# Kernel tuning notes

Hardware: AMD Instinct MI355X
Metric: run time of the kernel (lower is better)

## Reference

```python
import jax, jax.numpy as jnp
import numpy as np


def _gru_dir(x, kernel, rec_kernel, bias):
    """Keras GRU (reset_after=True). x: [B,T,D] -> [B,T,U]."""
    B, T, D = x.shape
    U = rec_kernel.shape[0]
    # Precompute input projections for all timesteps: [B,T,3U]
    xw = jnp.einsum('btd,dk->btk', x, kernel) + bias[0]
    h0 = jnp.zeros((B, U), dtype=x.dtype)

    def step(h, xw_t):
        rec = h @ rec_kernel + bias[1]            # [B,3U]
        xz, xr, xh = jnp.split(xw_t, 3, axis=-1)
        rz, rr, rh = jnp.split(rec, 3, axis=-1)
        z = jax.nn.sigmoid(xz + rz)
        r = jax.nn.sigmoid(xr + rr)
        hh = jnp.tanh(xh + r * rh)
        h_new = z * h + (1.0 - z) * hh
        return h_new, h_new

    _, hs = jax.lax.scan(step, h0, jnp.swapaxes(xw, 0, 1))  # hs: [T,B,U]
    return jnp.swapaxes(hs, 0, 1)


def setup_inputs() -> dict:
    key = jax.random.key(0)
    ks = jax.random.split(key, 7)
    B, T, D, U = 64, 1024, 256, 256
    s_in = 1.0 / np.sqrt(D)
    s_rec = 1.0 / np.sqrt(U)
    return {
        'x': jax.random.normal(ks[0], (B, T, D), jnp.float32),
        'kernel_f': jax.random.normal(ks[1], (D, 3 * U), jnp.float32) * s_in,
        'rec_kernel_f': jax.random.normal(ks[2], (U, 3 * U), jnp.float32) * s_rec,
        'bias_f': jnp.zeros((2, 3 * U), jnp.float32),
        'kernel_b': jax.random.normal(ks[3], (D, 3 * U), jnp.float32) * s_in,
        'rec_kernel_b': jax.random.normal(ks[4], (U, 3 * U), jnp.float32) * s_rec,
        'bias_b': jnp.zeros((2, 3 * U), jnp.float32),
    }


def reference(x, kernel_f, rec_kernel_f, bias_f, kernel_b, rec_kernel_b, bias_b):
    # Forward direction
    out_f = _gru_dir(x, kernel_f, rec_kernel_f, bias_f)
    # Backward direction: reverse time, run GRU, reverse output back
    xb = x[:, ::-1, :]
    out_b = _gru_dir(xb, kernel_b, rec_kernel_b, bias_b)[:, ::-1, :]
    # Bidirectional merge_mode='concat'
    return jnp.concatenate([out_f, out_b], axis=-1)  # [B,T,2U]
```

## Files before the change

### kernel.cpp

```cpp
#include <hip/hip_runtime.h>
#include <hip/hip_fp16.h>
#include <hip/hip_bf16.h>

typedef __attribute__((ext_vector_type(8))) short bf16x8;
typedef __attribute__((ext_vector_type(4))) float f32x4;

__device__ __forceinline__ short f2bf(float f) {
    unsigned u = __builtin_bit_cast(unsigned, f);
    unsigned r = (u + 0x7FFFu + ((u >> 16) & 1u)) >> 16;
    return (short)r;
}
__device__ __forceinline__ float fast_rcp(float x) {
    return __builtin_amdgcn_rcpf(x);
}
__device__ __forceinline__ float fast_exp(float x) {
    return __builtin_amdgcn_exp2f(x * 1.4426950408889634f);
}

__global__ __launch_bounds__(256) void prep_kernel(
    const float* __restrict__ kf, const float* __restrict__ kb,
    const float* __restrict__ rf, const float* __restrict__ rb,
    short* __restrict__ kT, short* __restrict__ rTf, short* __restrict__ rTb)
{
    int idx = blockIdx.x * 256 + threadIdx.x;
    int n = idx >> 8;
    int k = idx & 255;
    const float* src = (n < 768) ? kf : kb;
    int nn = (n < 768) ? n : (n - 768);
    kT[idx] = f2bf(src[k * 768 + nn]);
    if (n < 768) {
        rTf[idx] = f2bf(rf[k * 768 + n]);
        rTb[idx] = f2bf(rb[k * 768 + n]);
    }
}

__global__ __launch_bounds__(256) void proj_kernel(
    const float* __restrict__ x, const short* __restrict__ kT,
    const float* __restrict__ bias_f, const float* __restrict__ bias_b,
    char* __restrict__ xwp_f, char* __restrict__ xwp_b)
{
    __shared__ short lA[64][264];
    __shared__ short lB[128][264];

    const int tid = threadIdx.x;
    const int m0 = blockIdx.x * 64;
    const int n0 = blockIdx.y * 128;

    const int b_blk  = m0 >> 10;
    const int bg     = b_blk >> 4;
    const int rowg   = b_blk & 15;
    const int hi_t   = rowg >> 2;
    const int i_t    = rowg & 3;
    const int tbase  = m0 & 1023;

#pragma unroll
    for (int rep = 0; rep < 16; ++rep) {
        int lin = rep * 256 + tid;
        int r = lin >> 6;
        int c4 = lin & 63;
        float4 v = *(const float4*)(x + (size_t)(m0 + r) * 256 + c4 * 4);
        short4 s;
        s.x = f2bf(v.x); s.y = f2bf(v.y); s.z = f2bf(v.z); s.w = f2bf(v.w);
        *(short4*)&lA[r][c4 * 4] = s;
    }
#pragma unroll
    for (int rep = 0; rep < 16; ++rep) {
        int lin = rep * 256 + tid;
        int r = lin >> 5;
        int c8 = lin & 31;
        uint4 v = *(const uint4*)(kT + (size_t)(n0 + r) * 256 + c8 * 8);
        *(uint4*)&lB[r][c8 * 8] = v;
    }
    __syncthreads();

    const int w = tid >> 6, l = tid & 63;
    const int l15 = l & 15, hi = l >> 4;

    bf16x8 a[8];
#pragma unroll
    for (int kt = 0; kt < 8; ++kt)
        a[kt] = *(const bf16x8*)&lA[w * 16 + l15][kt * 32 + hi * 8];

#pragma unroll
    for (int j = 0; j < 8; ++j) {
        f32x4 acc = {0.f, 0.f, 0.f, 0.f};
#pragma unroll
        for (int kt = 0; kt < 8; ++kt) {
            bf16x8 b = *(const bf16x8*)&lB[j * 16 + l15][kt * 32 + hi * 8];
            acc = __builtin_amdgcn_mfma_f32_16x16x32_bf16(a[kt], b, acc, 0, 0, 0);
        }
        int ng = n0 + j * 16 + l15;
        int dirb = ng >= 768;
        int nn = ng - (dirb ? 768 : 0);
        const float* bias = dirb ? bias_b : bias_f;
        float badd = bias[nn] + ((nn < 512) ? bias[768 + nn] : 0.f);
        char* basep = dirb ? xwp_b : xwp_f;

        int g   = nn >> 8;
        int cg2 = nn & 255;
        int wt  = cg2 >> 4;
        int lane_t = hi_t * 16 + (cg2 & 15);

#pragma unroll
        for (int i = 0; i < 4; ++i) {
            int t = tbase + w * 16 + hi * 4 + i;
            unsigned short hv = __builtin_bit_cast(unsigned short,
                                    __float2half(acc[i] + badd));
            if (g < 2) {
                *(unsigned short*)(basep + ((size_t)bg << 24) + ((size_t)t << 14)
                                   + (wt << 10) + (lane_t << 4) + ((g * 4 + i_t) << 1)) = hv;
            } else {
                *(unsigned short*)(basep + 67108864u + ((size_t)bg << 23) + ((size_t)t << 13)
                                   + (wt << 9) + (lane_t << 3) + (i_t << 1)) = hv;
            }
        }
    }
}

#define GRU_STEP(PR, PW)                                                     \
  {                                                                          \
    uint4  xv16 = *(const uint4*)xp16;  xp16 += step16;                      \
    uint2  xv8  = *(const uint2*)xp8;   xp8  += step8;                       \
    unsigned bbase = 0;                                                      \
    asm volatile("" : "+v"(bbase));    \
    f32x4 az = {0.f,0.f,0.f,0.f}, ar = {0.f,0.f,0.f,0.f},                    \
          ah = {0.f,0.f,0.f,0.f};                                            \
    _Pragma("unroll") for (int kt = 0; kt < 8; ++kt) {                       \
      bf16x8 aq = *(const bf16x8*)((const char*)hfrag + (PR)*8192            \
                                   + kt * 1024 + l * 16);                    \
      bf16x8 bh;                                                             \
      if (kt < 5) bh = Bh[kt];                                               \
      else bh = *(const bf16x8*)((const char*)bfrag + bbase                  \
                                 + (kt - 5) * 16384 + w * 1024 + l * 16);    \
      az = __builtin_amdgcn_mfma_f32_16x16x32_bf16(aq, Bz[kt], az, 0,0,0);   \
      ar = __builtin_amdgcn_mfma_f32_16x16x32_bf16(aq, Br[kt], ar, 0,0,0);   \
      ah = __builtin_amdgcn_mfma_f32_16x16x32_bf16(aq, bh, ah, 0,0,0);       \
    }                                                                        \
    const __half* hx  = (const __half*)&xv16;                                \
    const __half* hx8 = (const __half*)&xv8;                                 \
    float hn[4];                                                             \
    _Pragma("unroll") for (int i = 0; i < 4; ++i) {                          \
      float zi  = fast_rcp(1.f + fast_exp(-(__half2float(hx[i]) + az[i])));  \
      float rri = fast_rcp(1.f + fast_exp(-(__half2float(hx[4+i]) + ar[i])));\
      float pre = __half2float(hx8[i]) + rri * (ah[i] + b1h);                \
      float sg  = fast_rcp(1.f + fast_exp(-2.f * pre));                      \
      float hh  = 2.f * sg - 1.f;                                            \
      float h2  = hh + zi * (hold[i] - hh);                                  \
      hold[i] = h2;  hn[i] = h2;                                             \
      opbase[i * 524288] = h2;                                               \
    }                                                                        \
    unsigned pk0, pk1;                                                       \
    asm("v_cvt_pk_bf16_f32 %0, %1, %2" : "=v"(pk0) : "v"(hn[0]), "v"(hn[1]));\
    asm("v_cvt_pk_bf16_f32 %0, %1, %2" : "=v"(pk1) : "v"(hn[2]), "v"(hn[3]));\
    {                                                                        \
      char* hb = (char*)hfrag + (PW)*8192 + wb;                              \
      *(short*)(hb)      = (short)(pk0 & 0xffff);                            \
      *(short*)(hb + 16) = (short)(pk0 >> 16);                               \
      *(short*)(hb + 32) = (short)(pk1 & 0xffff);                            \
      *(short*)(hb + 48) = (short)(pk1 >> 16);                               \
    }                                                                        \
    opbase += ostep;                                                         \
    asm volatile("s_waitcnt lgkmcnt(0)\n\ts_barrier" ::: "memory");          \
  }

__global__ __launch_bounds__(1024) void gru_kernel(
    const char* __restrict__ xwp_f, const char* __restrict__ xwp_b,
    const short* __restrict__ recT_f, const short* __restrict__ recT_b,
    const float* __restrict__ bias_f, const float* __restrict__ bias_b,
    float* __restrict__ out)
{
    __shared__ short hfrag[2][8][64][8];
    __shared__ short bfrag[3][16][64][8];

    const int tid = threadIdx.x;
    const int w = tid >> 6, l = tid & 63;
    const int l15 = l & 15, hi = l >> 4;
    const int dir = blockIdx.x >> 2;
    const int bg  = blockIdx.x & 3;
    const int b0  = bg * 16;

    const char*  xwp  = dir ? xwp_b  : xwp_f;
    const short* recT = dir ? recT_b : recT_f;
    const float* bias = dir ? bias_b : bias_f;

    const int cg = w * 16 + l15;
    const float b1h = bias[768 + 512 + cg];

    ((int4*)hfrag)[tid] = make_int4(0, 0, 0, 0);

    const char* recTc = (const char*)recT;
    unsigned offz = (((unsigned)(cg)       * 256u) + hi * 8u) * 2u;
    unsigned offr = (((unsigned)(256 + cg) * 256u) + hi * 8u) * 2u;
    unsigned offh = (((unsigned)(512 + cg) * 256u) + hi * 8u) * 2u;
    bf16x8 Bz[8], Br[8], Bh[5];
#pragma unroll
    for (int kt = 0; kt < 8; ++kt) {
        Bz[kt] = *(const bf16x8*)(recTc + offz + kt * 64);
        Br[kt] = *(const bf16x8*)(recTc + offr + kt * 64);
    }
#pragma unroll
    for (int kt = 0; kt < 5; ++kt)
        Bh[kt] = *(const bf16x8*)(recTc + offh + kt * 64);
#pragma unroll
    for (int kt = 5; kt < 8; ++kt) {
        bf16x8 tmp = *(const bf16x8*)(recTc + offh + kt * 64);
        *(bf16x8*)((char*)bfrag + (kt - 5) * 16384 + w * 1024 + l * 16) = tmp;
    }

    const int t0 = dir ? 1023 : 0;
    const long step16 = dir ? -16384 : 16384;
    const long step8  = dir ? -8192  : 8192;
    const char* xp16 = xwp + ((size_t)bg << 24) + ((size_t)t0 << 14)
                       + (w << 10) + (l << 4);
    const char* xp8  = xwp + 67108864u + ((size_t)bg << 23) + ((size_t)t0 << 13)
                       + (w << 9) + (l << 3);

    const long ostep = dir ? -512 : 512;
    float* opbase = out + (size_t)(b0 + hi * 4) * 524288 + (size_t)t0 * 512
                    + (size_t)dir * 256 + cg;

    const unsigned wb = (unsigned)(cg >> 5) * 1024u
                      + ((((unsigned)cg >> 3) & 3u) * 16u) * 16u
                      + (unsigned)(hi * 4) * 16u + ((unsigned)(l15 & 7)) * 2u;

    f32x4 hold = {0.f, 0.f, 0.f, 0.f};
    __syncthreads();

    for (int su = 0; su < 512; ++su) {
        GRU_STEP(0, 1)
        GRU_STEP(1, 0)
    }
}

extern "C" void kernel_launch(void* const* d_in, const int* in_sizes, int n_in,
                              void* d_out, int out_size, void* d_ws, size_t ws_size,
                              hipStream_t stream) {
    const float* x   = (const float*)d_in[0];
    const float* kf  = (const float*)d_in[1];
    const float* rf  = (const float*)d_in[2];
    const float* bf_ = (const float*)d_in[3];
    const float* kb  = (const float*)d_in[4];
    const float* rb  = (const float*)d_in[5];
    const float* bb_ = (const float*)d_in[6];

    char* ws = (char*)d_ws;
    char* xwp_f = ws;
    char* xwp_b = ws + 100663296;
    short* rTf  = (short*)(ws + 201326592);
    short* rTb  = (short*)(ws + 201719808);
    short* kT   = (short*)(ws + 202113024);
    float* out  = (float*)d_out;

    hipLaunchKernelGGL(prep_kernel, dim3(1536), dim3(256), 0, stream,
                       kf, kb, rf, rb, kT, rTf, rTb);
    hipLaunchKernelGGL(proj_kernel, dim3(1024, 12), dim3(256), 0, stream,
                       x, kT, bf_, bb_, xwp_f, xwp_b);
    hipLaunchKernelGGL(gru_kernel, dim3(8), dim3(1024), 0, stream,
                       xwp_f, xwp_b, rTf, rTb, bf_, bb_, out);
}
```

Baseline: 1.867 ms.

## Split each GRU recurrence across two workgroups exchanging hidden state via global flags

Each direction/batch-group recurrence now runs on two 512-thread workgroups, each owning half of the hidden units. The full recurrent weight slice sits in registers, which removes the LDS-staged weight fragments. Each step, a block publishes its bf16 half of h to global memory and raises an atomic flag. The partner spin-waits on that flag, then loads the other half of h for the remaining MFMAs. This halves per-block matmul work and doubles the number of CUs used, at the cost of a cross-CU global-memory handshake on every one of the 1024 serial steps.

New measurement: 4.594 ms. 146% more time.

```diff
diff --git a/kernel.cpp b/kernel.cpp
--- a/kernel.cpp
+++ b/kernel.cpp
@@ -117,28 +117,45 @@
     }
 }
 
-#define GRU_STEP(PR, PW)                                                     \
+#define GRU_STEP(PR, PW, RSLOT, PSLOT)                                       \
   {                                                                          \
     uint4  xv16 = *(const uint4*)xp16;  xp16 += step16;                      \
     uint2  xv8  = *(const uint2*)xp8;   xp8  += step8;                       \
-    unsigned bbase = 0;                                                      \
-    asm volatile("" : "+v"(bbase));    \
     f32x4 az = {0.f,0.f,0.f,0.f}, ar = {0.f,0.f,0.f,0.f},                    \
           ah = {0.f,0.f,0.f,0.f};                                            \
-    _Pragma("unroll") for (int kt = 0; kt < 8; ++kt) {                       \
-      bf16x8 aq = *(const bf16x8*)((const char*)hfrag + (PR)*8192            \
-                                   + kt * 1024 + l * 16);                    \
-      bf16x8 bh;                                                             \
-      if (kt < 5) bh = Bh[kt];                                               \
-      else bh = *(const bf16x8*)((const char*)bfrag + bbase                  \
-                                 + (kt - 5) * 16384 + w * 1024 + l * 16);    \
-      az = __builtin_amdgcn_mfma_f32_16x16x32_bf16(aq, Bz[kt], az, 0,0,0);   \
-      ar = __builtin_amdgcn_mfma_f32_16x16x32_bf16(aq, Br[kt], ar, 0,0,0);   \
-      ah = __builtin_amdgcn_mfma_f32_16x16x32_bf16(aq, bh, ah, 0,0,0);       \
+    _Pragma("unroll") for (int ko = 0; ko < 4; ++ko) {                       \
+      bf16x8 aq = *(const bf16x8*)((const char*)hfrag + (PR)*4096            \
+                                   + ko * 1024 + l * 16);                    \
+      az = __builtin_amdgcn_mfma_f32_16x16x32_bf16(aq, BzO[ko], az, 0,0,0);  \
+      ar = __builtin_amdgcn_mfma_f32_16x16x32_bf16(aq, BrO[ko], ar, 0,0,0);  \
+      ah = __builtin_amdgcn_mfma_f32_16x16x32_bf16(aq, BhO[ko], ah, 0,0,0);  \
+    }                                                                        \
+    if (s > 0) {                                                             \
+      while (__hip_atomic_load(flagp, __ATOMIC_ACQUIRE,                      \
+                               __HIP_MEMORY_SCOPE_AGENT) < s)                \
+        __builtin_amdgcn_s_sleep(1);                                         \
+      const char* rb = pubR + (RSLOT)*4096 + l15 * 256 + hi * 16;            \
+      bf16x8 ra0 = *(const bf16x8*)(rb);                                     \
+      bf16x8 ra1 = *(const bf16x8*)(rb + 64);                                \
+      bf16x8 ra2 = *(const bf16x8*)(rb + 128);                               \
+      bf16x8 ra3 = *(const bf16x8*)(rb + 192);                               \
+      az = __builtin_amdgcn_mfma_f32_16x16x32_bf16(ra0, BzR[0], az, 0,0,0);  \
+      ar = __builtin_amdgcn_mfma_f32_16x16x32_bf16(ra0, BrR[0], ar, 0,0,0);  \
+      ah = __builtin_amdgcn_mfma_f32_16x16x32_bf16(ra0, BhR[0], ah, 0,0,0);  \
+      az = __builtin_amdgcn_mfma_f32_16x16x32_bf16(ra1, BzR[1], az, 0,0,0);  \
+      ar = __builtin_amdgcn_mfma_f32_16x16x32_bf16(ra1, BrR[1], ar, 0,0,0);  \
+      ah = __builtin_amdgcn_mfma_f32_16x16x32_bf16(ra1, BhR[1], ah, 0,0,0);  \
+      az = __builtin_amdgcn_mfma_f32_16x16x32_bf16(ra2, BzR[2], az, 0,0,0);  \
+      ar = __builtin_amdgcn_mfma_f32_16x16x32_bf16(ra2, BrR[2], ar, 0,0,0);  \
+      ah = __builtin_amdgcn_mfma_f32_16x16x32_bf16(ra2, BhR[2], ah, 0,0,0);  \
+      az = __builtin_amdgcn_mfma_f32_16x16x32_bf16(ra3, BzR[3], az, 0,0,0);  \
+      ar = __builtin_amdgcn_mfma_f32_16x16x32_bf16(ra3, BrR[3], ar, 0,0,0);  \
+      ah = __builtin_amdgcn_mfma_f32_16x16x32_bf16(ra3, BhR[3], ah, 0,0,0);  \
     }                                                                        \
     const __half* hx  = (const __half*)&xv16;                                \
     const __half* hx8 = (const __half*)&xv8;                                 \
     float hn[4];                                                             \
+    char* pubw = pubMe + (PSLOT)*4096 + (hi * 4) * 256 + col_rel * 2;        \
     _Pragma("unroll") for (int i = 0; i < 4; ++i) {                          \
       float zi  = fast_rcp(1.f + fast_exp(-(__half2float(hx[i]) + az[i])));  \
       float rri = fast_rcp(1.f + fast_exp(-(__half2float(hx[4+i]) + ar[i])));\
@@ -148,42 +165,52 @@
       float h2  = hh + zi * (hold[i] - hh);                                  \
       hold[i] = h2;  hn[i] = h2;                                             \
       opbase[i * 524288] = h2;                                               \
+      *(short*)(pubw + i * 256) = f2bf(h2);                                  \
     }                                                                        \
     unsigned pk0, pk1;                                                       \
     asm("v_cvt_pk_bf16_f32 %0, %1, %2" : "=v"(pk0) : "v"(hn[0]), "v"(hn[1]));\
     asm("v_cvt_pk_bf16_f32 %0, %1, %2" : "=v"(pk1) : "v"(hn[2]), "v"(hn[3]));\
     {                                                                        \
-      char* hb = (char*)hfrag + (PW)*8192 + wb;                              \
+      char* hb = (char*)hfrag + (PW)*4096 + wb;                              \
       *(short*)(hb)      = (short)(pk0 & 0xffff);                            \
       *(short*)(hb + 16) = (short)(pk0 >> 16);                               \
       *(short*)(hb + 32) = (short)(pk1 & 0xffff);                            \
       *(short*)(hb + 48) = (short)(pk1 >> 16);                               \
     }                                                                        \
     opbase += ostep;                                                         \
-    asm volatile("s_waitcnt lgkmcnt(0)\n\ts_barrier" ::: "memory");          \
+    __syncthreads();              \
+    if (tid == 0)                                                            \
+      __hip_atomic_store(flagMe, s + 1, __ATOMIC_RELEASE,                    \
+                         __HIP_MEMORY_SCOPE_AGENT);                          \
+    ++s;                                                                     \
   }
 
-__global__ __launch_bounds__(1024) void gru_kernel(
+__global__ __launch_bounds__(512) void gru_kernel(
     const char* __restrict__ xwp_f, const char* __restrict__ xwp_b,
     const short* __restrict__ recT_f, const short* __restrict__ recT_b,
     const float* __restrict__ bias_f, const float* __restrict__ bias_b,
+    char* __restrict__ hpub, int* __restrict__ flags,
     float* __restrict__ out)
 {
-    __shared__ short hfrag[2][8][64][8];
-    __shared__ short bfrag[3][16][64][8];
+    __shared__ short hfrag[2][4][64][8];
 
     const int tid = threadIdx.x;
     const int w = tid >> 6, l = tid & 63;
     const int l15 = l & 15, hi = l >> 4;
-    const int dir = blockIdx.x >> 2;
-    const int bg  = blockIdx.x & 3;
-    const int b0  = bg * 16;
+    const int bid  = blockIdx.x;
+    const int half = bid >> 3;
+    const int dir  = (bid >> 2) & 1;
+    const int bg   = bid & 3;
+    const int b0   = bg * 16;
+    const int c0   = half * 128;
+    const int pbid = bid ^ 8;
 
     const char*  xwp  = dir ? xwp_b  : xwp_f;
     const short* recT = dir ? recT_b : recT_f;
     const float* bias = dir ? bias_b : bias_f;
 
-    const int cg = w * 16 + l15;
+    const int col_rel = w * 16 + l15;
+    const int cg = c0 + col_rel;
     const float b1h = bias[768 + 512 + cg];
 
     ((int4*)hfrag)[tid] = make_int4(0, 0, 0, 0);
@@ -192,43 +219,48 @@
     unsigned offz = (((unsigned)(cg)       * 256u) + hi * 8u) * 2u;
     unsigned offr = (((unsigned)(256 + cg) * 256u) + hi * 8u) * 2u;
     unsigned offh = (((unsigned)(512 + cg) * 256u) + hi * 8u) * 2u;
-    bf16x8 Bz[8], Br[8], Bh[5];
-#pragma unroll
-    for (int kt = 0; kt < 8; ++kt) {
-        Bz[kt] = *(const bf16x8*)(recTc + offz + kt * 64);
-        Br[kt] = *(const bf16x8*)(recTc + offr + kt * 64);
-    }
-#pragma unroll
-    for (int kt = 0; kt < 5; ++kt)
-        Bh[kt] = *(const bf16x8*)(recTc + offh + kt * 64);
-#pragma unroll
-    for (int kt = 5; kt < 8; ++kt) {
-        bf16x8 tmp = *(const bf16x8*)(recTc + offh + kt * 64);
-        *(bf16x8*)((char*)bfrag + (kt - 5) * 16384 + w * 1024 + l * 16) = tmp;
+    const int ktlo = half * 4;
+    const int ktro = 4 - ktlo;
+    bf16x8 BzO[4], BrO[4], BhO[4], BzR[4], BrR[4], BhR[4];
+#pragma unroll
+    for (int k = 0; k < 4; ++k) {
+        BzO[k] = *(const bf16x8*)(recTc + offz + (ktlo + k) * 64);
+        BrO[k] = *(const bf16x8*)(recTc + offr + (ktlo + k) * 64);
+        BhO[k] = *(const bf16x8*)(recTc + offh + (ktlo + k) * 64);
+        BzR[k] = *(const bf16x8*)(recTc + offz + (ktro + k) * 64);
+        BrR[k] = *(const bf16x8*)(recTc + offr + (ktro + k) * 64);
+        BhR[k] = *(const bf16x8*)(recTc + offh + (ktro + k) * 64);
     }
 
     const int t0 = dir ? 1023 : 0;
     const long step16 = dir ? -16384 : 16384;
     const long step8  = dir ? -8192  : 8192;
+    const int wt = half * 8 + w;
     const char* xp16 = xwp + ((size_t)bg << 24) + ((size_t)t0 << 14)
-                       + (w << 10) + (l << 4);
+                       + (wt << 10) + (l << 4);
     const char* xp8  = xwp + 67108864u + ((size_t)bg << 23) + ((size_t)t0 << 13)
-                       + (w << 9) + (l << 3);
+                       + (wt << 9) + (l << 3);
 
     const long ostep = dir ? -512 : 512;
     float* opbase = out + (size_t)(b0 + hi * 4) * 524288 + (size_t)t0 * 512
                     + (size_t)dir * 256 + cg;
 
-    const unsigned wb = (unsigned)(cg >> 5) * 1024u
-                      + ((((unsigned)cg >> 3) & 3u) * 16u) * 16u
-                      + (unsigned)(hi * 4) * 16u + ((unsigned)(l15 & 7)) * 2u;
+    const unsigned wb = (unsigned)(col_rel >> 5) * 1024u
+                      + (unsigned)((2 * w + (l15 >> 3)) & 3) * 256u
+                      + (unsigned)hi * 64u + (unsigned)(l15 & 7) * 2u;
+
+    char* pubMe = hpub + (size_t)bid * 8192;
+    const char* pubR = hpub + (size_t)pbid * 8192;
+    int* flagMe = flags + bid;
+    const int* flagp = flags + pbid;
 
     f32x4 hold = {0.f, 0.f, 0.f, 0.f};
+    int s = 0;
     __syncthreads();
 
     for (int su = 0; su < 512; ++su) {
-        GRU_STEP(0, 1)
-        GRU_STEP(1, 0)
+        GRU_STEP(0, 1, 0, 1)
+        GRU_STEP(1, 0, 1, 0)
     }
 }
 
@@ -249,12 +281,15 @@
     short* rTf  = (short*)(ws + 201326592);
     short* rTb  = (short*)(ws + 201719808);
     short* kT   = (short*)(ws + 202113024);
+    char*  hpub = ws + 202899456;
+    int*   flags = (int*)(ws + 203030528);
     float* out  = (float*)d_out;
 
+    hipMemsetAsync(flags, 0, 64, stream);
     hipLaunchKernelGGL(prep_kernel, dim3(1536), dim3(256), 0, stream,
                        kf, kb, rf, rb, kT, rTf, rTb);
     hipLaunchKernelGGL(proj_kernel, dim3(1024, 12), dim3(256), 0, stream,
                        x, kT, bf_, bb_, xwp_f, xwp_b);
-    hipLaunchKernelGGL(gru_kernel, dim3(8), dim3(1024), 0, stream,
-                       xwp_f, xwp_b, rTf, rTb, bf_, bb_, out);
-}
+    hipLaunchKernelGGL(gru_kernel, dim3(16), dim3(512), 0, stream,
+                       xwp_f, xwp_b, rTf, rTb, bf_, bb_, hpub, flags, out);
+}
```

## Halve GRU block to 512 threads with two column tiles per wave

Applied to the files above, without the earlier changes.

The recurrent kernel now launches 8 waves instead of 16, and each wave handles two 16-column tiles of the hidden state. It reuses the same A fragment (h) across six MFMAs per k-step and doubles the register-resident recurrent weights. The aim is to shrink the per-step barrier cost and cut redundant LDS reads of h, since fewer waves synchronise each timestep. The cost is much higher register pressure, which may cause spills, and more serial gate math per wave on the critical path.

Measured after the change: 1.939 ms. 1.04x slower.

```diff
diff --git a/kernel.cpp b/kernel.cpp
--- a/kernel.cpp
+++ b/kernel.cpp
@@ -117,60 +117,78 @@
     }
 }
 
-#define GRU_STEP(PR, PW)                                                     \
-  {                                                                          \
-    uint4  xv16 = *(const uint4*)xp16;  xp16 += step16;                      \
-    uint2  xv8  = *(const uint2*)xp8;   xp8  += step8;                       \
-    unsigned bbase = 0;                                                      \
-    asm volatile("" : "+v"(bbase));    \
-    f32x4 az = {0.f,0.f,0.f,0.f}, ar = {0.f,0.f,0.f,0.f},                    \
-          ah = {0.f,0.f,0.f,0.f};                                            \
-    _Pragma("unroll") for (int kt = 0; kt < 8; ++kt) {                       \
-      bf16x8 aq = *(const bf16x8*)((const char*)hfrag + (PR)*8192            \
-                                   + kt * 1024 + l * 16);                    \
-      bf16x8 bh;                                                             \
-      if (kt < 5) bh = Bh[kt];                                               \
-      else bh = *(const bf16x8*)((const char*)bfrag + bbase                  \
-                                 + (kt - 5) * 16384 + w * 1024 + l * 16);    \
-      az = __builtin_amdgcn_mfma_f32_16x16x32_bf16(aq, Bz[kt], az, 0,0,0);   \
-      ar = __builtin_amdgcn_mfma_f32_16x16x32_bf16(aq, Br[kt], ar, 0,0,0);   \
-      ah = __builtin_amdgcn_mfma_f32_16x16x32_bf16(aq, bh, ah, 0,0,0);       \
-    }                                                                        \
-    const __half* hx  = (const __half*)&xv16;                                \
-    const __half* hx8 = (const __half*)&xv8;                                 \
-    float hn[4];                                                             \
+#define MFMA_BF16(A, B, C) __builtin_amdgcn_mfma_f32_16x16x32_bf16(A, B, C, 0, 0, 0)
+
+#define GRU_GATES(AZ, AR, AH, HX, HX8, HOLD, OPOFF, WBOFF, B1H)              \
     _Pragma("unroll") for (int i = 0; i < 4; ++i) {                          \
-      float zi  = fast_rcp(1.f + fast_exp(-(__half2float(hx[i]) + az[i])));  \
-      float rri = fast_rcp(1.f + fast_exp(-(__half2float(hx[4+i]) + ar[i])));\
-      float pre = __half2float(hx8[i]) + rri * (ah[i] + b1h);                \
+      float zi  = fast_rcp(1.f + fast_exp(-(__half2float(HX[i]) + AZ[i])));  \
+      float rri = fast_rcp(1.f + fast_exp(-(__half2float(HX[4+i]) + AR[i])));\
+      float pre = __half2float(HX8[i]) + rri * (AH[i] + B1H);                \
       float sg  = fast_rcp(1.f + fast_exp(-2.f * pre));                      \
       float hh  = 2.f * sg - 1.f;                                            \
-      float h2  = hh + zi * (hold[i] - hh);                                  \
-      hold[i] = h2;  hn[i] = h2;                                             \
-      opbase[i * 524288] = h2;                                               \
+      float h2  = hh + zi * (HOLD[i] - hh);                                  \
+      HOLD[i] = h2;  hn[i] = h2;                                             \
+      opbase[(OPOFF) + i * 524288] = h2;                                     \
     }                                                                        \
-    unsigned pk0, pk1;                                                       \
     asm("v_cvt_pk_bf16_f32 %0, %1, %2" : "=v"(pk0) : "v"(hn[0]), "v"(hn[1]));\
     asm("v_cvt_pk_bf16_f32 %0, %1, %2" : "=v"(pk1) : "v"(hn[2]), "v"(hn[3]));\
     {                                                                        \
-      char* hb = (char*)hfrag + (PW)*8192 + wb;                              \
+      char* hb = hwBase + (WBOFF);                                           \
       *(short*)(hb)      = (short)(pk0 & 0xffff);                            \
       *(short*)(hb + 16) = (short)(pk0 >> 16);                               \
       *(short*)(hb + 32) = (short)(pk1 & 0xffff);                            \
       *(short*)(hb + 48) = (short)(pk1 >> 16);                               \
+    }
+
+#define GRU_STEP(PR, PW)                                                     \
+  {                                                                          \
+    uint4 xv16a = *(const uint4*)xp16;                                       \
+    uint4 xv16b = *(const uint4*)(xp16 + 1024);  xp16 += step16;             \
+    uint2 xv8a  = *(const uint2*)xp8;                                        \
+    uint2 xv8b  = *(const uint2*)(xp8 + 512);    xp8  += step8;              \
+    unsigned bb = 0;                                                         \
+    asm volatile("" : "+v"(bb));       \
+    f32x4 az0={0.f,0.f,0.f,0.f}, ar0={0.f,0.f,0.f,0.f}, ah0={0.f,0.f,0.f,0.f};\
+    f32x4 az1={0.f,0.f,0.f,0.f}, ar1={0.f,0.f,0.f,0.f}, ah1={0.f,0.f,0.f,0.f};\
+    _Pragma("unroll") for (int kt = 0; kt < 8; ++kt) {                       \
+      bf16x8 aq = *(const bf16x8*)((const char*)hfrag + (PR)*8192            \
+                                   + kt * 1024 + l * 16);                    \
+      bf16x8 bh0v, bh1v;                                                     \
+      if (kt < 5) { bh0v = Bh0[kt]; bh1v = Bh1[kt]; }                        \
+      else {                                                                 \
+        bh0v = *(const bf16x8*)(bfragc + bb + (kt - 5) * 8192                \
+                                + w * 1024 + l * 16);                        \
+        bh1v = *(const bf16x8*)(bfragc + bb + 24576 + (kt - 5) * 8192        \
+                                + w * 1024 + l * 16);                        \
+      }                                                                      \
+      az0 = MFMA_BF16(aq, Bz0[kt], az0);                                     \
+      ar0 = MFMA_BF16(aq, Br0[kt], ar0);                                     \
+      ah0 = MFMA_BF16(aq, bh0v,    ah0);                                     \
+      az1 = MFMA_BF16(aq, Bz1[kt], az1);                                     \
+      ar1 = MFMA_BF16(aq, Br1[kt], ar1);                                     \
+      ah1 = MFMA_BF16(aq, bh1v,    ah1);                                     \
     }                                                                        \
+    const __half* hxa  = (const __half*)&xv16a;                              \
+    const __half* hx8a = (const __half*)&xv8a;                               \
+    const __half* hxb  = (const __half*)&xv16b;                              \
+    const __half* hx8b = (const __half*)&xv8b;                               \
+    float hn[4];                                                             \
+    unsigned pk0, pk1;                                                       \
+    char* hwBase = (char*)hfrag + (PW)*8192;                                 \
+    GRU_GATES(az0, ar0, ah0, hxa, hx8a, hold0, 0,  wb,       b1h0)           \
+    GRU_GATES(az1, ar1, ah1, hxb, hx8b, hold1, 16, wb + 512, b1h1)           \
     opbase += ostep;                                                         \
     asm volatile("s_waitcnt lgkmcnt(0)\n\ts_barrier" ::: "memory");          \
   }
 
-__global__ __launch_bounds__(1024) void gru_kernel(
+__global__ __launch_bounds__(512) void gru_kernel(
     const char* __restrict__ xwp_f, const char* __restrict__ xwp_b,
     const short* __restrict__ recT_f, const short* __restrict__ recT_b,
     const float* __restrict__ bias_f, const float* __restrict__ bias_b,
     float* __restrict__ out)
 {
     __shared__ short hfrag[2][8][64][8];
-    __shared__ short bfrag[3][16][64][8];
+    __shared__ short bfrag[2][3][8][64][8];
 
     const int tid = threadIdx.x;
     const int w = tid >> 6, l = tid & 63;
@@ -183,47 +201,57 @@
     const short* recT = dir ? recT_b : recT_f;
     const float* bias = dir ? bias_b : bias_f;
 
-    const int cg = w * 16 + l15;
-    const float b1h = bias[768 + 512 + cg];
-
-    ((int4*)hfrag)[tid] = make_int4(0, 0, 0, 0);
+    const int cg0 = w * 32 + l15;
+    const float b1h0 = bias[768 + 512 + cg0];
+    const float b1h1 = bias[768 + 512 + cg0 + 16];
+
+    ((int4*)hfrag)[tid]       = make_int4(0, 0, 0, 0);
+    ((int4*)hfrag)[tid + 512] = make_int4(0, 0, 0, 0);
 
     const char* recTc = (const char*)recT;
-    unsigned offz = (((unsigned)(cg)       * 256u) + hi * 8u) * 2u;
-    unsigned offr = (((unsigned)(256 + cg) * 256u) + hi * 8u) * 2u;
-    unsigned offh = (((unsigned)(512 + cg) * 256u) + hi * 8u) * 2u;
-    bf16x8 Bz[8], Br[8], Bh[5];
+    const char* bfragc = (const char*)bfrag;
+    unsigned offz = (((unsigned)(cg0)       * 256u) + hi * 8u) * 2u;
+    unsigned offr = (((unsigned)(256 + cg0) * 256u) + hi * 8u) * 2u;
+    unsigned offh = (((unsigned)(512 + cg0) * 256u) + hi * 8u) * 2u;
+    bf16x8 Bz0[8], Br0[8], Bz1[8], Br1[8], Bh0[5], Bh1[5];
 #pragma unroll
     for (int kt = 0; kt < 8; ++kt) {
-        Bz[kt] = *(const bf16x8*)(recTc + offz + kt * 64);
-        Br[kt] = *(const bf16x8*)(recTc + offr + kt * 64);
-    }
-#pragma unroll
-    for (int kt = 0; kt < 5; ++kt)
-        Bh[kt] = *(const bf16x8*)(recTc + offh + kt * 64);
+        Bz0[kt] = *(const bf16x8*)(recTc + offz + kt * 64);
+        Br0[kt] = *(const bf16x8*)(recTc + offr + kt * 64);
+        Bz1[kt] = *(const bf16x8*)(recTc + offz + 8192 + kt * 64);
+        Br1[kt] = *(const bf16x8*)(recTc + offr + 8192 + kt * 64);
+    }
+#pragma unroll
+    for (int kt = 0; kt < 5; ++kt) {
+        Bh0[kt] = *(const bf16x8*)(recTc + offh + kt * 64);
+        Bh1[kt] = *(const bf16x8*)(recTc + offh + 8192 + kt * 64);
+    }
 #pragma unroll
     for (int kt = 5; kt < 8; ++kt) {
-        bf16x8 tmp = *(const bf16x8*)(recTc + offh + kt * 64);
-        *(bf16x8*)((char*)bfrag + (kt - 5) * 16384 + w * 1024 + l * 16) = tmp;
+        bf16x8 t0v = *(const bf16x8*)(recTc + offh + kt * 64);
+        bf16x8 t1v = *(const bf16x8*)(recTc + offh + 8192 + kt * 64);
+        *(bf16x8*)((char*)bfrag + (kt - 5) * 8192 + w * 1024 + l * 16) = t0v;
+        *(bf16x8*)((char*)bfrag + 24576 + (kt - 5) * 8192 + w * 1024 + l * 16) = t1v;
     }
 
     const int t0 = dir ? 1023 : 0;
     const long step16 = dir ? -16384 : 16384;
     const long step8  = dir ? -8192  : 8192;
     const char* xp16 = xwp + ((size_t)bg << 24) + ((size_t)t0 << 14)
-                       + (w << 10) + (l << 4);
+                       + ((2 * w) << 10) + (l << 4);
     const char* xp8  = xwp + 67108864u + ((size_t)bg << 23) + ((size_t)t0 << 13)
-                       + (w << 9) + (l << 3);
+                       + ((2 * w) << 9) + (l << 3);
 
     const long ostep = dir ? -512 : 512;
     float* opbase = out + (size_t)(b0 + hi * 4) * 524288 + (size_t)t0 * 512
-                    + (size_t)dir * 256 + cg;
-
-    const unsigned wb = (unsigned)(cg >> 5) * 1024u
-                      + ((((unsigned)cg >> 3) & 3u) * 16u) * 16u
-                      + (unsigned)(hi * 4) * 16u + ((unsigned)(l15 & 7)) * 2u;
-
-    f32x4 hold = {0.f, 0.f, 0.f, 0.f};
+                    + (size_t)dir * 256 + cg0;
+
+    const unsigned wb = (unsigned)(cg0 >> 5) * 1024u
+                      + (unsigned)((cg0 >> 3) & 3) * 256u
+                      + (unsigned)(hi * 4) * 16u + (unsigned)(cg0 & 7) * 2u;
+
+    f32x4 hold0 = {0.f, 0.f, 0.f, 0.f};
+    f32x4 hold1 = {0.f, 0.f, 0.f, 0.f};
     __syncthreads();
 
     for (int su = 0; su < 512; ++su) {
@@ -255,6 +283,6 @@
                        kf, kb, rf, rb, kT, rTf, rTb);
     hipLaunchKernelGGL(proj_kernel, dim3(1024, 12), dim3(256), 0, stream,
                        x, kT, bf_, bb_, xwp_f, xwp_b);
-    hipLaunchKernelGGL(gru_kernel, dim3(8), dim3(1024), 0, stream,
+    hipLaunchKernelGGL(gru_kernel, dim3(8), dim3(512), 0, stream,
                        xwp_f, xwp_b, rTf, rTb, bf_, bb_, out);
 }
```
